# Kernel optimization log

Hardware: AMD Instinct MI355X
Metric: run time of the kernel (lower is better)

Reference implementation:

```python
import jax, jax.numpy as jnp
import numpy as np

B, D_IN, H, D_OUT = 4096, 4096, 2048, 1000
LN_EPS = 1e-5


def setup_inputs() -> dict:
    key = jax.random.key(0)
    ks = jax.random.split(key, 8)
    s_in = 1.0 / np.sqrt(H)  # torch RNN init: U(-1/sqrt(H), 1/sqrt(H))
    inp = {
        "x": jax.random.normal(ks[0], (B, D_IN), dtype=jnp.float32),
        "W_ih0": jax.random.uniform(ks[1], (H, D_IN), jnp.float32, -s_in, s_in),
        "b_ih0": jax.random.uniform(ks[2], (H,), jnp.float32, -s_in, s_in),
        "b_hh0": jax.random.uniform(ks[3], (H,), jnp.float32, -s_in, s_in),
        "W_ih1": jax.random.uniform(ks[4], (H, H), jnp.float32, -s_in, s_in),
        "b_ih1": jax.random.uniform(ks[5], (H,), jnp.float32, -s_in, s_in),
        "b_hh1": jax.random.uniform(ks[6], (H,), jnp.float32, -s_in, s_in),
        "ln_g": jnp.ones((2 * H,), jnp.float32),
        "ln_b": jnp.zeros((2 * H,), jnp.float32),
        "fc_W": jax.random.uniform(ks[7], (D_OUT, 2 * H), jnp.float32, -1.0 / np.sqrt(2 * H), 1.0 / np.sqrt(2 * H)),
        "fc_b": jnp.zeros((D_OUT,), jnp.float32),
    }
    return inp


def reference(x, W_ih0, b_ih0, b_hh0, W_ih1, b_ih1, b_hh1, ln_g, ln_b, fc_W, fc_b):
    # seq_len == 1, h0 == 0 -> W_hh terms vanish; only biases remain.
    h1 = jnp.tanh(x @ W_ih0.T + b_ih0 + b_hh0)          # [B, H]
    h2 = jnp.tanh(h1 @ W_ih1.T + b_ih1 + b_hh1)         # [B, H]
    # last_hidden == mean_pooled (single step) -> concat duplicates h2
    combined = jnp.concatenate([h2, h2], axis=1)        # [B, 2H]
    mu = combined.mean(axis=-1, keepdims=True)
    var = combined.var(axis=-1, keepdims=True)
    normed = (combined - mu) * jax.lax.rsqrt(var + LN_EPS) * ln_g + ln_b
    # dropout is identity in eval mode
    return normed @ fc_W.T + fc_b                        # [B, D_OUT]
```

## Files before the change

kernel.cpp:

```cpp
#include <hip/hip_runtime.h>
#include <hip/hip_bf16.h>

typedef __attribute__((ext_vector_type(8))) unsigned short ushort8;
typedef __attribute__((ext_vector_type(8))) __bf16 bf16x8;
typedef __attribute__((ext_vector_type(4))) float f32x4;
typedef __attribute__((ext_vector_type(4))) float floatx4;

__device__ __forceinline__ unsigned short f2bf(float f) {
    unsigned u = __builtin_bit_cast(unsigned, f);
    u += 0x7fffu + ((u >> 16) & 1u);
    return (unsigned short)(u >> 16);
}
__device__ __forceinline__ float bf2f(unsigned short h) {
    unsigned u = ((unsigned)h) << 16;
    return __builtin_bit_cast(float, u);
}

__device__ __forceinline__ void gload_lds16(const void* g, void* l) {
    __builtin_amdgcn_global_load_lds(
        (const __attribute__((address_space(1))) void*)g,
        (__attribute__((address_space(3))) void*)l,
        16, 0, 0);
}

#define BAR()      asm volatile("s_barrier" ::: "memory")

__global__ __launch_bounds__(256) void cvt_f2bf(const float* __restrict__ in,
                                                unsigned short* __restrict__ out,
                                                int n8) {
    int i = blockIdx.x * 256 + threadIdx.x;
    if (i >= n8) return;
    floatx4 a = ((const floatx4*)in)[2 * i];
    floatx4 b = ((const floatx4*)in)[2 * i + 1];
    ushort8 o;
#pragma unroll
    for (int j = 0; j < 4; ++j) { o[j] = f2bf(a[j]); o[4 + j] = f2bf(b[j]); }
    ((ushort8*)out)[i] = o;
}

__global__ __launch_bounds__(256) void weff_kernel(const float* __restrict__ fcW,
                                                   const float* __restrict__ lng,
                                                   const float* __restrict__ lnb,
                                                   const float* __restrict__ fcb,
                                                   unsigned short* __restrict__ weff,
                                                   float* __restrict__ cc) {
    int o = blockIdx.x;
    int tid = threadIdx.x;
    if (o >= 1000) {
        ushort8 z = {0, 0, 0, 0, 0, 0, 0, 0};
        ((ushort8*)(weff + (size_t)o * 2048))[tid] = z;
        if (tid == 0) cc[o] = 0.f;
        return;
    }
    const float* wrow = fcW + (size_t)o * 4096;
    int j0 = tid * 8;
    floatx4 wa  = *(const floatx4*)(wrow + j0);
    floatx4 wb  = *(const floatx4*)(wrow + j0 + 4);
    floatx4 wa2 = *(const floatx4*)(wrow + 2048 + j0);
    floatx4 wb2 = *(const floatx4*)(wrow + 2048 + j0 + 4);
    floatx4 ga  = *(const floatx4*)(lng + j0);
    floatx4 gb  = *(const floatx4*)(lng + j0 + 4);
    floatx4 ga2 = *(const floatx4*)(lng + 2048 + j0);
    floatx4 gb2 = *(const floatx4*)(lng + 2048 + j0 + 4);
    floatx4 ba  = *(const floatx4*)(lnb + j0);
    floatx4 bb  = *(const floatx4*)(lnb + j0 + 4);
    floatx4 ba2 = *(const floatx4*)(lnb + 2048 + j0);
    floatx4 bb2 = *(const floatx4*)(lnb + 2048 + j0 + 4);
    ushort8 o8;
    float acc = 0.f;
#pragma unroll
    for (int j = 0; j < 4; ++j) {
        o8[j] = f2bf(ga[j] * wa[j] + ga2[j] * wa2[j]);
        acc += ba[j] * wa[j] + ba2[j] * wa2[j];
        o8[4 + j] = f2bf(gb[j] * wb[j] + gb2[j] * wb2[j]);
        acc += bb[j] * wb[j] + bb2[j] * wb2[j];
    }
    ((ushort8*)(weff + (size_t)o * 2048))[tid] = o8;
#pragma unroll
    for (int d = 32; d; d >>= 1) acc += __shfl_down(acc, d);
    __shared__ float red[4];
    if ((tid & 63) == 0) red[tid >> 6] = acc;
    __syncthreads();
    if (tid == 0) cc[o] = fcb[o] + red[0] + red[1] + red[2] + red[3];
}

__global__ __launch_bounds__(256) void ln_kernel(const unsigned short* __restrict__ h2,
                                                 unsigned short* __restrict__ z) {
    int row = blockIdx.x, tid = threadIdx.x;
    ushort8 v = ((const ushort8*)(h2 + (size_t)row * 2048))[tid];
    float f[8];
    float s = 0.f, s2 = 0.f;
#pragma unroll
    for (int j = 0; j < 8; ++j) { f[j] = bf2f(v[j]); s += f[j]; s2 += f[j] * f[j]; }
#pragma unroll
    for (int d = 32; d; d >>= 1) { s += __shfl_down(s, d); s2 += __shfl_down(s2, d); }
    __shared__ float rs_[4], rs2_[4];
    if ((tid & 63) == 0) { rs_[tid >> 6] = s; rs2_[tid >> 6] = s2; }
    __syncthreads();
    float S = rs_[0] + rs_[1] + rs_[2] + rs_[3];
    float S2 = rs2_[0] + rs2_[1] + rs2_[2] + rs2_[3];
    float mu = S * (1.f / 2048.f);
    float var = S2 * (1.f / 2048.f) - mu * mu;
    float r = rsqrtf(var + 1e-5f);
    ushort8 o;
#pragma unroll
    for (int j = 0; j < 8; ++j) o[j] = f2bf((f[j] - mu) * r);
    ((ushort8*)(z + (size_t)row * 2048))[tid] = o;
}

template <int EPI, int NJ>
__global__ __launch_bounds__(512, 2) void gemm_fr(const unsigned short* __restrict__ A,
                                                  const unsigned short* __restrict__ B,
                                                  int M, int N, int K,
                                                  const float* __restrict__ bias0,
                                                  const float* __restrict__ bias1,
                                                  void* __restrict__ Cout, int ncols) {
    extern __shared__ char smem[];
    constexpr int BUFSZ = 16384 + NJ * 8192;
    const int tid = threadIdx.x;
    const int lane = tid & 63, wid = tid >> 6;
    const int wm = wid >> 2, wn = wid & 3;
    const int fr = lane & 15, g = lane >> 4;

    const int nwg = gridDim.x * gridDim.y;
    const int fid = blockIdx.y * gridDim.x + blockIdx.x;
    const int cpx = nwg >> 3;
    const int sw = (fid & 7) * cpx + (fid >> 3);
    const int bx = sw % gridDim.x, by = sw / gridDim.x;
    const int row0 = by * 128, col0 = bx * (64 * NJ);

    const int tg = tid >> 3;
    const int tcE = ((tid & 7) ^ (tg & 7)) * 8;

    auto stageA = [&](int kt, char* buf) {
#pragma unroll
        for (int r = 0; r < 2; ++r)
            gload_lds16(A + (size_t)(row0 + r * 64 + tg) * K + kt * 64 + tcE,
                        buf + r * 8192 + wid * 1024);
    };
    auto stageB = [&](int kt, char* buf) {
#pragma unroll
        for (int rr = 0; rr < NJ; ++rr)
            gload_lds16(B + (size_t)(col0 + rr * 64 + tg) * K + kt * 64 + tcE,
                        buf + 16384 + rr * 8192 + wid * 1024);
    };

    const int xorv = (fr & 7) << 4;
    auto rdA = [&](const char* buf, int m, int kh) -> bf16x8 {
        int byte = (wm * 64 + m * 16 + fr) * 128 + ((kh * 64 + g * 16) ^ xorv);
        return __builtin_bit_cast(bf16x8, *(const ushort8*)(buf + byte));
    };
    auto rdB = [&](const char* buf, int n, int kh) -> bf16x8 {
        int byte = 16384 + (wn * (16 * NJ) + n * 16 + fr) * 128 + ((kh * 64 + g * 16) ^ xorv);
        return __builtin_bit_cast(bf16x8, *(const ushort8*)(buf + byte));
    };

    f32x4 acc[4][NJ];
#pragma unroll
    for (int i = 0; i < 4; ++i)
#pragma unroll
        for (int j = 0; j < NJ; ++j) acc[i][j] = f32x4{0.f, 0.f, 0.f, 0.f};

    char* p0 = smem;
    char* p1 = smem + BUFSZ;
    char* p2 = smem + 2 * BUFSZ;
    stageA(0, p0); stageB(0, p0);
    stageA(1, p1); stageB(1, p1);

    const int NT = K >> 6;
    for (int t = 0; t < NT; ++t) {
        char* rb = p0;
        char* wb = p2;
        if (t < NT - 1) {
            if constexpr (NJ == 4) asm volatile("s_waitcnt vmcnt(6)" ::: "memory");
            else                   asm volatile("s_waitcnt vmcnt(4)" ::: "memory");
        } else {
            asm volatile("s_waitcnt vmcnt(0)" ::: "memory");
        }
        BAR();
        if (t + 2 < NT) { stageA(t + 2, wb); stageB(t + 2, wb); }

        bf16x8 aF[4][2], bF[NJ][2];
#pragma unroll
        for (int m = 0; m < 4; ++m)
#pragma unroll
            for (int kh = 0; kh < 2; ++kh) aF[m][kh] = rdA(rb, m, kh);
#pragma unroll
        for (int n = 0; n < NJ; ++n)
#pragma unroll
            for (int kh = 0; kh < 2; ++kh) bF[n][kh] = rdB(rb, n, kh);

        __builtin_amdgcn_s_setprio(1);
#pragma unroll
        for (int m = 0; m < 4; ++m)
#pragma unroll
            for (int n = 0; n < NJ; ++n)
#pragma unroll
                for (int kh = 0; kh < 2; ++kh)
                    acc[m][n] = __builtin_amdgcn_mfma_f32_16x16x32_bf16(aF[m][kh], bF[n][kh], acc[m][n], 0, 0, 0);
        __builtin_amdgcn_s_setprio(0);

        char* tmp = p0; p0 = p1; p1 = p2; p2 = tmp;
    }

#pragma unroll
    for (int i = 0; i < 4; ++i) {
        int rbase = row0 + wm * 64 + i * 16 + g * 4;
#pragma unroll
        for (int j = 0; j < NJ; ++j) {
            int col = col0 + wn * (16 * NJ) + j * 16 + fr;
            if (EPI == 0) {
                float bsum = bias0[col] + bias1[col];
                unsigned short* O = (unsigned short*)Cout;
#pragma unroll
                for (int r = 0; r < 4; ++r)
                    O[(size_t)(rbase + r) * N + col] = f2bf(tanhf(acc[i][j][r] + bsum));
            } else {
                if (col < ncols) {
                    float bsum = bias0[col];
                    float* O = (float*)Cout;
#pragma unroll
                    for (int r = 0; r < 4; ++r)
                        O[(size_t)(rbase + r) * ncols + col] = acc[i][j][r] + bsum;
                }
            }
        }
    }
}

extern "C" void kernel_launch(void* const* d_in, const int* in_sizes, int n_in,
                              void* d_out, int out_size, void* d_ws, size_t ws_size,
                              hipStream_t stream) {
    const float* x   = (const float*)d_in[0];
    const float* W0  = (const float*)d_in[1];
    const float* bi0 = (const float*)d_in[2];
    const float* bh0 = (const float*)d_in[3];
    const float* W1  = (const float*)d_in[4];
    const float* bi1 = (const float*)d_in[5];
    const float* bh1 = (const float*)d_in[6];
    const float* lng = (const float*)d_in[7];
    const float* lnb = (const float*)d_in[8];
    const float* fcW = (const float*)d_in[9];
    const float* fcb = (const float*)d_in[10];
    float* out = (float*)d_out;

    char* w = (char*)d_ws;
    unsigned short* xb   = (unsigned short*)(w);
    unsigned short* w0b  = (unsigned short*)(w + 33554432ull);
    unsigned short* w1b  = (unsigned short*)(w + 50331648ull);
    unsigned short* h1   = (unsigned short*)(w + 58720256ull);
    unsigned short* h2   = (unsigned short*)(w + 75497472ull);
    unsigned short* zb   = (unsigned short*)(w + 92274688ull);
    unsigned short* weff = (unsigned short*)(w + 109051904ull);
    float* cc            = (float*)(w + 113246208ull);

    const int SHM0 = 3 * (16384 + 4 * 8192);
    const int SHM1 = 3 * (16384 + 2 * 8192);
    (void)hipFuncSetAttribute((const void*)gemm_fr<0, 4>,
                              hipFuncAttributeMaxDynamicSharedMemorySize, SHM0);
    (void)hipFuncSetAttribute((const void*)gemm_fr<1, 2>,
                              hipFuncAttributeMaxDynamicSharedMemorySize, SHM1);

    cvt_f2bf<<<8192, 256, 0, stream>>>(x,  xb,  2097152);
    cvt_f2bf<<<4096, 256, 0, stream>>>(W0, w0b, 1048576);
    cvt_f2bf<<<2048, 256, 0, stream>>>(W1, w1b, 524288);
    weff_kernel<<<1024, 256, 0, stream>>>(fcW, lng, lnb, fcb, weff, cc);
    gemm_fr<0, 4><<<dim3(8, 32), 512, SHM0, stream>>>(xb, w0b, 4096, 2048, 4096, bi0, bh0, h1, 2048);
    gemm_fr<0, 4><<<dim3(8, 32), 512, SHM0, stream>>>(h1, w1b, 4096, 2048, 2048, bi1, bh1, h2, 2048);
    ln_kernel<<<4096, 256, 0, stream>>>(h2, zb);
    gemm_fr<1, 2><<<dim3(8, 32), 512, SHM1, stream>>>(zb, weff, 4096, 1024, 2048, cc, nullptr, out, 1000);
}
```

Measured before the change: 174.2 us.

## Fold LayerNorm into final GEMM epilogue and deepen GEMM pipeline to four stages

The LayerNorm kernel now only writes per-row mean and rstd, and the final GEMM reads raw h2 directly. Its epilogue applies rstd*(acc - mu*colsum(Weff)) + c, using column sums computed in weff_kernel, which removes the write and reread of the normalized z tensor. The GEMM is also restructured to K-tiles of 32 with a 4-buffer ring and double-buffered register fragments, so LDS fragment reads for the next tile overlap the MFMAs of the current one. Risks are smaller per-stage tiles giving more barriers per unit of work, and a numeric difference from subtracting mu*wsum after bf16 accumulation.

```diff
diff --git a/kernel.cpp b/kernel.cpp
--- a/kernel.cpp
+++ b/kernel.cpp
@@ -23,7 +23,9 @@
         16, 0, 0);
 }
 
-#define BAR()      asm volatile("s_barrier" ::: "memory")
+#define BAR()   asm volatile("s_barrier" ::: "memory")
+#define VMW(n)  asm volatile("s_waitcnt vmcnt(" #n ")" ::: "memory")
+#define LGK(n)  asm volatile("s_waitcnt lgkmcnt(" #n ")" ::: "memory")
 
 __global__ __launch_bounds__(256) void cvt_f2bf(const float* __restrict__ in,
                                                 unsigned short* __restrict__ out,
@@ -43,13 +45,14 @@
                                                    const float* __restrict__ lnb,
                                                    const float* __restrict__ fcb,
                                                    unsigned short* __restrict__ weff,
-                                                   float* __restrict__ cc) {
+                                                   float* __restrict__ cc,
+                                                   float* __restrict__ wsum) {
     int o = blockIdx.x;
     int tid = threadIdx.x;
     if (o >= 1000) {
         ushort8 z = {0, 0, 0, 0, 0, 0, 0, 0};
         ((ushort8*)(weff + (size_t)o * 2048))[tid] = z;
-        if (tid == 0) cc[o] = 0.f;
+        if (tid == 0) { cc[o] = 0.f; wsum[o] = 0.f; }
         return;
     }
     const float* wrow = fcW + (size_t)o * 4096;
@@ -67,56 +70,60 @@
     floatx4 ba2 = *(const floatx4*)(lnb + 2048 + j0);
     floatx4 bb2 = *(const floatx4*)(lnb + 2048 + j0 + 4);
     ushort8 o8;
-    float acc = 0.f;
+    float acc = 0.f, ws = 0.f;
 #pragma unroll
     for (int j = 0; j < 4; ++j) {
         o8[j] = f2bf(ga[j] * wa[j] + ga2[j] * wa2[j]);
         acc += ba[j] * wa[j] + ba2[j] * wa2[j];
+        ws  += bf2f(o8[j]);
         o8[4 + j] = f2bf(gb[j] * wb[j] + gb2[j] * wb2[j]);
         acc += bb[j] * wb[j] + bb2[j] * wb2[j];
+        ws  += bf2f(o8[4 + j]);
     }
     ((ushort8*)(weff + (size_t)o * 2048))[tid] = o8;
 #pragma unroll
-    for (int d = 32; d; d >>= 1) acc += __shfl_down(acc, d);
-    __shared__ float red[4];
-    if ((tid & 63) == 0) red[tid >> 6] = acc;
+    for (int d = 32; d; d >>= 1) { acc += __shfl_down(acc, d); ws += __shfl_down(ws, d); }
+    __shared__ float red[4], redw[4];
+    if ((tid & 63) == 0) { red[tid >> 6] = acc; redw[tid >> 6] = ws; }
     __syncthreads();
-    if (tid == 0) cc[o] = fcb[o] + red[0] + red[1] + red[2] + red[3];
-}
-
-__global__ __launch_bounds__(256) void ln_kernel(const unsigned short* __restrict__ h2,
-                                                 unsigned short* __restrict__ z) {
+    if (tid == 0) {
+        cc[o] = fcb[o] + red[0] + red[1] + red[2] + red[3];
+        wsum[o] = redw[0] + redw[1] + redw[2] + redw[3];
+    }
+}
+
+__global__ __launch_bounds__(256) void ln_stats(const unsigned short* __restrict__ h2,
+                                                float2* __restrict__ mur) {
     int row = blockIdx.x, tid = threadIdx.x;
     ushort8 v = ((const ushort8*)(h2 + (size_t)row * 2048))[tid];
-    float f[8];
     float s = 0.f, s2 = 0.f;
 #pragma unroll
-    for (int j = 0; j < 8; ++j) { f[j] = bf2f(v[j]); s += f[j]; s2 += f[j] * f[j]; }
+    for (int j = 0; j < 8; ++j) { float f = bf2f(v[j]); s += f; s2 += f * f; }
 #pragma unroll
     for (int d = 32; d; d >>= 1) { s += __shfl_down(s, d); s2 += __shfl_down(s2, d); }
     __shared__ float rs_[4], rs2_[4];
     if ((tid & 63) == 0) { rs_[tid >> 6] = s; rs2_[tid >> 6] = s2; }
     __syncthreads();
-    float S = rs_[0] + rs_[1] + rs_[2] + rs_[3];
-    float S2 = rs2_[0] + rs2_[1] + rs2_[2] + rs2_[3];
-    float mu = S * (1.f / 2048.f);
-    float var = S2 * (1.f / 2048.f) - mu * mu;
-    float r = rsqrtf(var + 1e-5f);
-    ushort8 o;
-#pragma unroll
-    for (int j = 0; j < 8; ++j) o[j] = f2bf((f[j] - mu) * r);
-    ((ushort8*)(z + (size_t)row * 2048))[tid] = o;
+    if (tid == 0) {
+        float S = rs_[0] + rs_[1] + rs_[2] + rs_[3];
+        float S2 = rs2_[0] + rs2_[1] + rs2_[2] + rs2_[3];
+        float mu = S * (1.f / 2048.f);
+        float var = S2 * (1.f / 2048.f) - mu * mu;
+        mur[row] = make_float2(mu, rsqrtf(var + 1e-5f));
+    }
 }
 
 template <int EPI, int NJ>
-__global__ __launch_bounds__(512, 2) void gemm_fr(const unsigned short* __restrict__ A,
+__global__ __launch_bounds__(512, 2) void gemm_p2(const unsigned short* __restrict__ A,
                                                   const unsigned short* __restrict__ B,
                                                   int M, int N, int K,
                                                   const float* __restrict__ bias0,
                                                   const float* __restrict__ bias1,
-                                                  void* __restrict__ Cout, int ncols) {
+                                                  void* __restrict__ Cout, int ncols,
+                                                  const float2* __restrict__ mur,
+                                                  const float* __restrict__ wsum) {
     extern __shared__ char smem[];
-    constexpr int BUFSZ = 16384 + NJ * 8192;
+    constexpr int BUFSZ = 8192 + NJ * 4096;
     const int tid = threadIdx.x;
     const int lane = tid & 63, wid = tid >> 6;
     const int wm = wid >> 2, wn = wid & 3;
@@ -129,99 +136,107 @@
     const int bx = sw % gridDim.x, by = sw / gridDim.x;
     const int row0 = by * 128, col0 = bx * (64 * NJ);
 
-    const int tg = tid >> 3;
-    const int tcE = ((tid & 7) ^ (tg & 7)) * 8;
-
-    auto stageA = [&](int kt, char* buf) {
-#pragma unroll
-        for (int r = 0; r < 2; ++r)
-            gload_lds16(A + (size_t)(row0 + r * 64 + tg) * K + kt * 64 + tcE,
-                        buf + r * 8192 + wid * 1024);
+    const int srow = tid >> 2;
+    const int scole = (((tid & 3) << 4) ^ ((srow & 3) << 4)) >> 1;
+
+    auto stage = [&](int kt, char* buf) {
+        gload_lds16(A + (size_t)(row0 + srow) * K + kt * 32 + scole, buf + tid * 16);
+#pragma unroll
+        for (int rr = 0; rr < NJ / 2; ++rr)
+            gload_lds16(B + (size_t)(col0 + rr * 128 + srow) * K + kt * 32 + scole,
+                        buf + 8192 + rr * 8192 + tid * 16);
     };
-    auto stageB = [&](int kt, char* buf) {
-#pragma unroll
-        for (int rr = 0; rr < NJ; ++rr)
-            gload_lds16(B + (size_t)(col0 + rr * 64 + tg) * K + kt * 64 + tcE,
-                        buf + 16384 + rr * 8192 + wid * 1024);
+
+    const int kbyte = (g * 16) ^ ((fr & 3) << 4);
+    auto readFrags = [&](bf16x8 (&fa)[4], bf16x8 (&fb)[NJ], const char* buf) {
+#pragma unroll
+        for (int m = 0; m < 4; ++m)
+            fa[m] = __builtin_bit_cast(bf16x8,
+                *(const ushort8*)(buf + (wm * 64 + m * 16 + fr) * 64 + kbyte));
+#pragma unroll
+        for (int n = 0; n < NJ; ++n)
+            fb[n] = __builtin_bit_cast(bf16x8,
+                *(const ushort8*)(buf + 8192 + (wn * (16 * NJ) + n * 16 + fr) * 64 + kbyte));
     };
 
-    const int xorv = (fr & 7) << 4;
-    auto rdA = [&](const char* buf, int m, int kh) -> bf16x8 {
-        int byte = (wm * 64 + m * 16 + fr) * 128 + ((kh * 64 + g * 16) ^ xorv);
-        return __builtin_bit_cast(bf16x8, *(const ushort8*)(buf + byte));
+    f32x4 acc[4][NJ];
+#pragma unroll
+    for (int i = 0; i < 4; ++i)
+#pragma unroll
+        for (int j = 0; j < NJ; ++j) acc[i][j] = f32x4{0.f, 0.f, 0.f, 0.f};
+
+    auto domfma = [&](bf16x8 (&fa)[4], bf16x8 (&fb)[NJ]) {
+        __builtin_amdgcn_s_setprio(1);
+#pragma unroll
+        for (int m = 0; m < 4; ++m)
+#pragma unroll
+            for (int n = 0; n < NJ; ++n)
+                acc[m][n] = __builtin_amdgcn_mfma_f32_16x16x32_bf16(fa[m], fb[n], acc[m][n], 0, 0, 0);
+        __builtin_amdgcn_s_setprio(0);
     };
-    auto rdB = [&](const char* buf, int n, int kh) -> bf16x8 {
-        int byte = 16384 + (wn * (16 * NJ) + n * 16 + fr) * 128 + ((kh * 64 + g * 16) ^ xorv);
-        return __builtin_bit_cast(bf16x8, *(const ushort8*)(buf + byte));
-    };
-
-    f32x4 acc[4][NJ];
-#pragma unroll
-    for (int i = 0; i < 4; ++i)
-#pragma unroll
-        for (int j = 0; j < NJ; ++j) acc[i][j] = f32x4{0.f, 0.f, 0.f, 0.f};
-
-    char* p0 = smem;
-    char* p1 = smem + BUFSZ;
-    char* p2 = smem + 2 * BUFSZ;
-    stageA(0, p0); stageB(0, p0);
-    stageA(1, p1); stageB(1, p1);
-
-    const int NT = K >> 6;
-    for (int t = 0; t < NT; ++t) {
-        char* rb = p0;
-        char* wb = p2;
-        if (t < NT - 1) {
-            if constexpr (NJ == 4) asm volatile("s_waitcnt vmcnt(6)" ::: "memory");
-            else                   asm volatile("s_waitcnt vmcnt(4)" ::: "memory");
-        } else {
-            asm volatile("s_waitcnt vmcnt(0)" ::: "memory");
-        }
+
+    auto waitL = [&]() { if constexpr (NJ == 4) VMW(3); else VMW(2); };
+    auto guard = [&]() { if constexpr (NJ == 4) LGK(8); else LGK(6); };
+
+    char* q0 = smem;
+    char* q1 = smem + BUFSZ;
+    char* q2 = smem + 2 * BUFSZ;
+    char* q3 = smem + 3 * BUFSZ;
+
+    bf16x8 faA[4], fbA[NJ], faB[4], fbB[NJ];
+
+    stage(0, q0); stage(1, q1); stage(2, q2);
+    if constexpr (NJ == 4) VMW(6); else VMW(4);
+    BAR();
+    readFrags(faA, fbA, q0);
+
+    const int NT = K >> 5;
+    for (int t = 0; t < NT; t += 2) {
+        if (t + 2 < NT) waitL(); else VMW(0);
+        guard();
         BAR();
-        if (t + 2 < NT) { stageA(t + 2, wb); stageB(t + 2, wb); }
-
-        bf16x8 aF[4][2], bF[NJ][2];
-#pragma unroll
-        for (int m = 0; m < 4; ++m)
-#pragma unroll
-            for (int kh = 0; kh < 2; ++kh) aF[m][kh] = rdA(rb, m, kh);
-#pragma unroll
-        for (int n = 0; n < NJ; ++n)
-#pragma unroll
-            for (int kh = 0; kh < 2; ++kh) bF[n][kh] = rdB(rb, n, kh);
-
-        __builtin_amdgcn_s_setprio(1);
-#pragma unroll
-        for (int m = 0; m < 4; ++m)
-#pragma unroll
-            for (int n = 0; n < NJ; ++n)
-#pragma unroll
-                for (int kh = 0; kh < 2; ++kh)
-                    acc[m][n] = __builtin_amdgcn_mfma_f32_16x16x32_bf16(aF[m][kh], bF[n][kh], acc[m][n], 0, 0, 0);
-        __builtin_amdgcn_s_setprio(0);
-
-        char* tmp = p0; p0 = p1; p1 = p2; p2 = tmp;
+        if (t + 3 < NT) stage(t + 3, q3);
+        readFrags(faB, fbB, q1);
+        domfma(faA, fbA);
+        { char* tmp = q0; q0 = q1; q1 = q2; q2 = q3; q3 = tmp; }
+
+        if (t + 3 < NT) waitL(); else VMW(0);
+        guard();
+        BAR();
+        if (t + 4 < NT) stage(t + 4, q3);
+        if (t + 2 < NT) readFrags(faA, fbA, q1);
+        domfma(faB, fbB);
+        { char* tmp = q0; q0 = q1; q1 = q2; q2 = q3; q3 = tmp; }
     }
 
 #pragma unroll
     for (int i = 0; i < 4; ++i) {
         int rbase = row0 + wm * 64 + i * 16 + g * 4;
-#pragma unroll
-        for (int j = 0; j < NJ; ++j) {
-            int col = col0 + wn * (16 * NJ) + j * 16 + fr;
-            if (EPI == 0) {
+        if (EPI == 0) {
+#pragma unroll
+            for (int j = 0; j < NJ; ++j) {
+                int col = col0 + wn * (16 * NJ) + j * 16 + fr;
                 float bsum = bias0[col] + bias1[col];
                 unsigned short* O = (unsigned short*)Cout;
 #pragma unroll
                 for (int r = 0; r < 4; ++r)
                     O[(size_t)(rbase + r) * N + col] = f2bf(tanhf(acc[i][j][r] + bsum));
-            } else {
+            }
+        } else {
+            float2 mr[4];
+#pragma unroll
+            for (int r = 0; r < 4; ++r) mr[r] = mur[rbase + r];
+#pragma unroll
+            for (int j = 0; j < NJ; ++j) {
+                int col = col0 + wn * (16 * NJ) + j * 16 + fr;
                 if (col < ncols) {
-                    float bsum = bias0[col];
+                    float ws = wsum[col];
+                    float ccv = bias0[col];
                     float* O = (float*)Cout;
 #pragma unroll
                     for (int r = 0; r < 4; ++r)
-                        O[(size_t)(rbase + r) * ncols + col] = acc[i][j][r] + bsum;
+                        O[(size_t)(rbase + r) * ncols + col] =
+                            mr[r].y * (acc[i][j][r] - mr[r].x * ws) + ccv;
                 }
             }
         }
@@ -250,23 +265,27 @@
     unsigned short* w1b  = (unsigned short*)(w + 50331648ull);
     unsigned short* h1   = (unsigned short*)(w + 58720256ull);
     unsigned short* h2   = (unsigned short*)(w + 75497472ull);
-    unsigned short* zb   = (unsigned short*)(w + 92274688ull);
-    unsigned short* weff = (unsigned short*)(w + 109051904ull);
-    float* cc            = (float*)(w + 113246208ull);
-
-    const int SHM0 = 3 * (16384 + 4 * 8192);
-    const int SHM1 = 3 * (16384 + 2 * 8192);
-    (void)hipFuncSetAttribute((const void*)gemm_fr<0, 4>,
+    unsigned short* weff = (unsigned short*)(w + 92274688ull);
+    float* cc            = (float*)(w + 96468992ull);
+    float* wsum          = (float*)(w + 96473088ull);
+    float2* mur          = (float2*)(w + 96477184ull);
+
+    const int SHM0 = 4 * (8192 + 4 * 4096);
+    const int SHM1 = 4 * (8192 + 2 * 4096);
+    (void)hipFuncSetAttribute((const void*)gemm_p2<0, 4>,
                               hipFuncAttributeMaxDynamicSharedMemorySize, SHM0);
-    (void)hipFuncSetAttribute((const void*)gemm_fr<1, 2>,
+    (void)hipFuncSetAttribute((const void*)gemm_p2<1, 2>,
                               hipFuncAttributeMaxDynamicSharedMemorySize, SHM1);
 
     cvt_f2bf<<<8192, 256, 0, stream>>>(x,  xb,  2097152);
     cvt_f2bf<<<4096, 256, 0, stream>>>(W0, w0b, 1048576);
     cvt_f2bf<<<2048, 256, 0, stream>>>(W1, w1b, 524288);
-    weff_kernel<<<1024, 256, 0, stream>>>(fcW, lng, lnb, fcb, weff, cc);
-    gemm_fr<0, 4><<<dim3(8, 32), 512, SHM0, stream>>>(xb, w0b, 4096, 2048, 4096, bi0, bh0, h1, 2048);
-    gemm_fr<0, 4><<<dim3(8, 32), 512, SHM0, stream>>>(h1, w1b, 4096, 2048, 2048, bi1, bh1, h2, 2048);
-    ln_kernel<<<4096, 256, 0, stream>>>(h2, zb);
-    gemm_fr<1, 2><<<dim3(8, 32), 512, SHM1, stream>>>(zb, weff, 4096, 1024, 2048, cc, nullptr, out, 1000);
-}
+    weff_kernel<<<1024, 256, 0, stream>>>(fcW, lng, lnb, fcb, weff, cc, wsum);
+    gemm_p2<0, 4><<<dim3(8, 32), 512, SHM0, stream>>>(xb, w0b, 4096, 2048, 4096,
+                                                      bi0, bh0, h1, 2048, nullptr, nullptr);
+    gemm_p2<0, 4><<<dim3(8, 32), 512, SHM0, stream>>>(h1, w1b, 4096, 2048, 2048,
+                                                      bi1, bh1, h2, 2048, nullptr, nullptr);
+    ln_stats<<<4096, 256, 0, stream>>>(h2, mur);
+    gemm_p2<1, 2><<<dim3(8, 32), 512, SHM1, stream>>>(h2, weff, 4096, 1024, 2048,
+                                                      cc, nullptr, out, 1000, mur, wsum);
+}
```

Result: slower. 194.4 us (+11.6%).
